# Optimization experiments

Hardware: AMD Instinct MI355X
Metric: run time of the kernel (lower is better)

Reference implementation:

```python
import jax, jax.numpy as jnp
import numpy as np
import math

B, T, H, NH, L = 8, 256, 128, 2, 2
DH = H // NH
KC = 3
ITEMNUM = 50000
TIME_SPAN = 256
PERIODS = jnp.array([86400.0, 604800.0, 2592000.0], dtype=jnp.float32)
SCALE_MAGS = [1.0, 1.0, 1.0]
NEG = -1e9


def layernorm(x, g, b, eps=1e-8):
    mu = x.mean(-1, keepdims=True)
    var = ((x - mu) ** 2).mean(-1, keepdims=True)
    return (x - mu) / jnp.sqrt(var + eps) * g + b


def time_encode(t, time_proj):
    # HarmonicTimeEncoding: [sin(2*pi*t/c), cos(2*pi*t/c)] per cycle -> Linear(2K->H, no bias)
    phase = 2.0 * math.pi * t[..., None] / PERIODS
    enc = jnp.concatenate([jnp.sin(phase), jnp.cos(phase)], axis=-1)  # (..., 2K)
    return enc @ time_proj.T


def phase_bias_fn(t, lambdas):
    # PhaseSimilarityBias: per-cycle cosine similarity of (sin,cos) phase vectors
    phase = 2.0 * math.pi * t[..., None] / PERIODS  # (B,T,K)
    phi = jnp.stack([jnp.sin(phase), jnp.cos(phase)], axis=-1)  # (B,T,K,2)
    phi = phi / jnp.maximum(jnp.linalg.norm(phi, axis=-1, keepdims=True), 1e-12)
    sim = jnp.einsum('btkd,bskd->btsk', phi, phi)
    return (sim * lambdas).sum(-1)  # (B,T,T)


def setup_inputs() -> dict:
    key = jax.random.key(0)
    ks = jax.random.split(key, 40)
    def n(i, shape, std=0.02):
        return jax.random.normal(ks[i], shape, dtype=jnp.float32) * std
    inp = {}
    inp['log_seqs'] = jax.random.randint(ks[0], (B, T), 0, ITEMNUM + 1)
    inp['time_matrices'] = jax.random.randint(ks[1], (B, T, T), 0, TIME_SPAN + 1)
    inp['time_seq'] = jnp.sort(jax.random.uniform(ks[2], (B, T), dtype=jnp.float32) * 5e6, axis=-1)
    inp['pos_seqs'] = jax.random.randint(ks[3], (B, T), 1, ITEMNUM + 1)
    inp['neg_seqs'] = jax.random.randint(ks[4], (B, T), 1, ITEMNUM + 1)
    inp['target_times'] = jax.random.uniform(ks[5], (B,), dtype=jnp.float32) * 5e6
    inp['item_emb'] = n(6, (ITEMNUM + 1, H)).at[0].set(0.0)  # padding_idx=0
    inp['abs_pos_K'] = n(7, (T, H))
    inp['abs_pos_V'] = n(8, (T, H))
    inp['time_K_emb'] = n(9, (TIME_SPAN + 1, H))
    inp['time_V_emb'] = n(10, (TIME_SPAN + 1, H))
    inp['Wq'] = n(11, (L, H, H), 0.05); inp['bq'] = jnp.zeros((L, H))
    inp['Wk'] = n(12, (L, H, H), 0.05); inp['bk'] = jnp.zeros((L, H))
    inp['Wv'] = n(13, (L, H, H), 0.05); inp['bv'] = jnp.zeros((L, H))
    inp['attn_ln_g'] = jnp.ones((L, H)); inp['attn_ln_b'] = jnp.zeros((L, H))
    inp['fwd_ln_g'] = jnp.ones((L, H)); inp['fwd_ln_b'] = jnp.zeros((L, H))
    inp['w1'] = n(14, (L, H, H), 0.05); inp['b1'] = jnp.zeros((L, H))
    inp['w2'] = n(15, (L, H, H), 0.05); inp['b2'] = jnp.zeros((L, H))
    inp['last_ln_g'] = jnp.ones((H,)); inp['last_ln_b'] = jnp.zeros((H,))
    inp['time_proj'] = n(16, (H, 2 * KC), 1.0 / math.sqrt(H))
    inp['lambdas'] = jnp.array(SCALE_MAGS, dtype=jnp.float32)
    inp['pred_W'] = n(17, (H, H), 0.05)
    inp['fus_W1'] = n(18, (H, 2 * H), 0.05); inp['fus_b1'] = jnp.zeros((H,))
    inp['fus_W2'] = n(19, (H, H), 0.05); inp['fus_b2'] = jnp.zeros((H,))
    return inp


def reference(log_seqs, time_matrices, time_seq, pos_seqs, neg_seqs, target_times,
              item_emb, abs_pos_K, abs_pos_V, time_K_emb, time_V_emb,
              Wq, bq, Wk, bk, Wv, bv, attn_ln_g, attn_ln_b, fwd_ln_g, fwd_ln_b,
              w1, b1, w2, b2, last_ln_g, last_ln_b, time_proj, lambdas,
              pred_W, fus_W1, fus_b1, fus_W2, fus_b2):
    seqs = item_emb[log_seqs] * math.sqrt(H)
    seqs = seqs + time_encode(time_seq, time_proj)
    tl_mask = (log_seqs == 0)  # (B,T) padding mask
    keep = (~tl_mask)[..., None].astype(seqs.dtype)
    seqs = seqs * keep
    absK = abs_pos_K.reshape(T, NH, DH).transpose(1, 0, 2)  # (NH,T,DH)
    absV = abs_pos_V.reshape(T, NH, DH).transpose(1, 0, 2)
    tK = time_K_emb[time_matrices].reshape(B, T, T, NH, DH)  # (B,T,T,NH,DH)
    tV = time_V_emb[time_matrices].reshape(B, T, T, NH, DH)
    pbias = phase_bias_fn(time_seq, lambdas)  # (B,T,T)
    causal = jnp.triu(jnp.ones((T, T), dtype=bool), k=1)
    mask = causal[None, None] | tl_mask[:, None, None, :]  # (B,1,T,T)
    for l in range(L):
        Qn = layernorm(seqs, attn_ln_g[l], attn_ln_b[l])
        q = (Qn @ Wq[l].T + bq[l]).reshape(B, T, NH, DH).transpose(0, 2, 1, 3)
        k = (seqs @ Wk[l].T + bk[l]).reshape(B, T, NH, DH).transpose(0, 2, 1, 3)
        v = (seqs @ Wv[l].T + bv[l]).reshape(B, T, NH, DH).transpose(0, 2, 1, 3)
        scores = jnp.einsum('bhqd,bhkd->bhqk', q, k)
        scores = scores + jnp.einsum('bhqd,hkd->bhqk', q, absK)
        scores = scores + jnp.einsum('bqkhd,bhqd->bhqk', tK, q)  # relative time-interval term
        scores = scores / math.sqrt(DH) + pbias[:, None]  # phase-similarity logit bias
        scores = jnp.where(mask, NEG, scores)
        A = jax.nn.softmax(scores, axis=-1)
        out = jnp.einsum('bhqk,bhkd->bhqd', A, v)
        out = out + jnp.einsum('bhqk,hkd->bhqd', A, absV)
        out = out + jnp.einsum('bhqk,bqkhd->bhqd', A, tV)
        out = out.transpose(0, 2, 1, 3).reshape(B, T, H)
        seqs = Qn + out
        x = layernorm(seqs, fwd_ln_g[l], fwd_ln_b[l])
        seqs = jax.nn.relu(x @ w1[l].T + b1[l]) @ w2[l].T + b2[l] + x
        seqs = seqs * keep
    log_feats = layernorm(seqs, last_ln_g, last_ln_b)
    H_per = time_encode(target_times, time_proj) @ pred_W.T  # (B,H)
    H_per = jnp.broadcast_to(H_per[:, None], (B, T, H))
    cat = jnp.concatenate([log_feats, H_per], axis=-1)
    fused = jax.nn.gelu(cat @ fus_W1.T + fus_b1, approximate=False) @ fus_W2.T + fus_b2
    pos_logits = (fused * item_emb[pos_seqs]).sum(-1)
    neg_logits = (fused * item_emb[neg_seqs]).sum(-1)
    return (pos_logits, neg_logits)
```

## Files before the change

### kernel.cpp

```cpp
#include <hip/hip_runtime.h>
#include <math.h>

#define TT 256
#define HH 128

__device__ __forceinline__ void enc6(float t, float e[6]) {
  float x = 6.2831853071795864769f * t;
  float a0 = x / 86400.0f, a1 = x / 604800.0f, a2 = x / 2592000.0f;
  e[0] = sinf(a0); e[1] = sinf(a1); e[2] = sinf(a2);
  e[3] = cosf(a0); e[4] = cosf(a1); e[5] = cosf(a2);
}

__global__ __launch_bounds__(128) void embed_kernel(
    const int* __restrict__ log_seqs, const float* __restrict__ time_seq,
    const float* __restrict__ item_emb, const float* __restrict__ time_proj,
    float* __restrict__ seqs, float* __restrict__ sc6) {
  int row = blockIdx.x;
  int h = threadIdx.x;
  float t = time_seq[row];
  float e[6]; enc6(t, e);
  int idx = log_seqs[row];
  const float* tp = time_proj + h * 6;
  float val = item_emb[(size_t)idx * HH + h] * 11.313708498984761f;
  val += e[0]*tp[0] + e[1]*tp[1] + e[2]*tp[2] + e[3]*tp[3] + e[4]*tp[4] + e[5]*tp[5];
  seqs[(size_t)row * HH + h] = (idx != 0) ? val : 0.0f;
  if (h < 6) sc6[row * 6 + h] = e[h];
}

__global__ __launch_bounds__(128) void qkv_fused(
    const float* __restrict__ S,
    const float* __restrict__ Wq, const float* __restrict__ bq,
    const float* __restrict__ Wk, const float* __restrict__ bk,
    const float* __restrict__ Wv, const float* __restrict__ bv,
    const float* __restrict__ lng, const float* __restrict__ lnb,
    const float* __restrict__ absK, const float* __restrict__ absV,
    float* __restrict__ QN, float* __restrict__ QB,
    float* __restrict__ KT, float* __restrict__ VB) {
  int which = blockIdx.x >> 8;
  int m0 = (blockIdx.x & 255) * 8;
  int n = threadIdx.x;
  __shared__ float At[8][132];
  __shared__ float mu[8], rs[8];
  #pragma unroll
  for (int r = 0; r < 8; ++r) At[r][n] = S[(size_t)(m0 + r) * HH + n];
  __syncthreads();
  if (which == 0) {
    if (n < 64) {
      int r = n >> 3, sg = n & 7;
      float s = 0.f;
      #pragma unroll
      for (int i = 0; i < 16; ++i) s += At[r][sg * 16 + i];
      s += __shfl_xor(s, 1); s += __shfl_xor(s, 2); s += __shfl_xor(s, 4);
      if (sg == 0) mu[r] = s * (1.0f / HH);
    }
    __syncthreads();
    if (n < 64) {
      int r = n >> 3, sg = n & 7;
      float mm = mu[r], s = 0.f;
      #pragma unroll
      for (int i = 0; i < 16; ++i) { float d = At[r][sg*16+i] - mm; s += d * d; }
      s += __shfl_xor(s, 1); s += __shfl_xor(s, 2); s += __shfl_xor(s, 4);
      if (sg == 0) rs[r] = rsqrtf(s * (1.0f / HH) + 1e-8f);
    }
    __syncthreads();
    float gg = lng[n], bb = lnb[n];
    #pragma unroll
    for (int r = 0; r < 8; ++r) {
      float v = (At[r][n] - mu[r]) * rs[r] * gg + bb;
      At[r][n] = v;
      QN[(size_t)(m0 + r) * HH + n] = v;
    }
    __syncthreads();
  }
  const float* W    = which == 0 ? Wq : which == 1 ? Wk : Wv;
  const float* bias = which == 0 ? bq : which == 1 ? bk : bv;
  const float* addP = which == 1 ? absK : which == 2 ? absV : nullptr;
  float* dst        = which == 0 ? QB : which == 1 ? KT : VB;
  float acc[8];
  #pragma unroll
  for (int r = 0; r < 8; ++r) acc[r] = 0.f;
  const float* wr = W + (size_t)n * HH;
  for (int d = 0; d < HH; d += 4) {
    float4 w = *(const float4*)(wr + d);
    #pragma unroll
    for (int r = 0; r < 8; ++r) {
      float4 a = *(const float4*)(&At[r][d]);
      acc[r] = fmaf(a.x, w.x, fmaf(a.y, w.y, fmaf(a.z, w.z, fmaf(a.w, w.w, acc[r]))));
    }
  }
  float bn = bias[n];
  #pragma unroll
  for (int r = 0; r < 8; ++r) {
    int m = m0 + r;
    float v = acc[r] + bn;
    if (addP) v += addP[(size_t)(m & 255) * HH + n];
    if (which == 1) {
      int bb2 = m >> 8, t = m & 255, hh2 = n >> 6, dd = n & 63;
      dst[(((size_t)(bb2 * 2 + hh2) * 64) + dd) * 256 + t] = v;
    } else {
      dst[(size_t)m * HH + n] = v;
    }
  }
}

__global__ __launch_bounds__(256) void pkscb_kernel(
    const float* __restrict__ QB, const float* __restrict__ tKe,
    const int* __restrict__ tmat, const int* __restrict__ log_seqs,
    const float* __restrict__ sc6, const float* __restrict__ lambdas,
    float* __restrict__ SCB) {
  int blk = blockIdx.x;
  int qt = blk & 63, bh = blk >> 6;
  int h = bh & 1, b = bh >> 1;
  int q0 = qt << 2, hoff = h << 6;
  int tid = threadIdx.x;
  __shared__ float Qs[4][64];
  __shared__ float PKl[4][264];
  __shared__ float sk6T[6][256];
  __shared__ float sq6[4][6];
  __shared__ unsigned char kmask[256];
  { int q = tid >> 6, d = tid & 63;
    Qs[q][d] = QB[((size_t)(b * TT + q0 + q)) * HH + hoff + d]; }
  for (int idx = tid; idx < 1536; idx += 256) {
    int kk = idx / 6, cc = idx - kk * 6;
    sk6T[cc][kk] = sc6[(size_t)b * 1536 + idx];
  }
  if (tid < 24) {
    int q = tid / 6, cc = tid - q * 6;
    sq6[q][cc] = sc6[((size_t)(b * TT + q0 + q)) * 6 + cc];
  }
  kmask[tid] = (log_seqs[b * TT + tid] == 0) ? 1 : 0;
  __syncthreads();
  for (int i = tid; i < 257; i += 256) {
    const float* tp = tKe + (size_t)i * HH + hoff;
    float a0 = 0.f, a1 = 0.f, a2 = 0.f, a3 = 0.f;
    #pragma unroll
    for (int d = 0; d < 64; d += 4) {
      float4 t4 = *(const float4*)(tp + d);
      float4 v0 = *(const float4*)(&Qs[0][d]);
      float4 v1 = *(const float4*)(&Qs[1][d]);
      float4 v2 = *(const float4*)(&Qs[2][d]);
      float4 v3 = *(const float4*)(&Qs[3][d]);
      a0 = fmaf(v0.x,t4.x,fmaf(v0.y,t4.y,fmaf(v0.z,t4.z,fmaf(v0.w,t4.w,a0))));
      a1 = fmaf(v1.x,t4.x,fmaf(v1.y,t4.y,fmaf(v1.z,t4.z,fmaf(v1.w,t4.w,a1))));
      a2 = fmaf(v2.x,t4.x,fmaf(v2.y,t4.y,fmaf(v2.z,t4.z,fmaf(v2.w,t4.w,a2))));
      a3 = fmaf(v3.x,t4.x,fmaf(v3.y,t4.y,fmaf(v3.z,t4.z,fmaf(v3.w,t4.w,a3))));
    }
    PKl[0][i] = a0 * 0.125f; PKl[1][i] = a1 * 0.125f;
    PKl[2][i] = a2 * 0.125f; PKl[3][i] = a3 * 0.125f;
  }
  __syncthreads();
  float l0 = lambdas[0], l1 = lambdas[1], l2 = lambdas[2];
  int k = tid;
  float c0 = sk6T[0][k], c1 = sk6T[1][k], c2 = sk6T[2][k],
        c3 = sk6T[3][k], c4 = sk6T[4][k], c5 = sk6T[5][k];
  int km = kmask[k];
  float* scbq = SCB + ((size_t)(bh * TT + q0)) * TT;
  #pragma unroll
  for (int qq = 0; qq < 4; ++qq) {
    int qg = q0 + qq;
    float pb = l0 * (sq6[qq][0] * c0 + sq6[qq][3] * c3)
             + l1 * (sq6[qq][1] * c1 + sq6[qq][4] * c4)
             + l2 * (sq6[qq][2] * c2 + sq6[qq][5] * c5);
    int tm = tmat[((size_t)(b * TT + qg)) * TT + k];
    float val = (k > qg || km) ? -1e9f : (PKl[qq][tm] + pb);
    scbq[(size_t)qq * TT + k] = val;
  }
}

__global__ __launch_bounds__(256) void attn_fused(
    const float* __restrict__ QB, const float* __restrict__ KT,
    const float* __restrict__ VB, const float* __restrict__ QN,
    const float* __restrict__ SCB, const int* __restrict__ tmat,
    const float* __restrict__ tVe, float* __restrict__ out) {
  int blk = blockIdx.x;
  blk = (blk & 7) * 256 + (blk >> 3);
  int qt = blk & 127;
  int h = (blk >> 7) & 1;
  int b = blk >> 8;
  int q0 = qt << 1;
  int hoff = h << 6;
  int tid = threadIdx.x;
  int w = tid >> 6, lane = tid & 63;

  __shared__ float Qt[2][64];
  __shared__ float Pp[2][256];
  __shared__ unsigned short tmq[2][256];
  __shared__ float part[4][2][64];
  __shared__ float red[16];

  if (tid < 128)
    Qt[tid >> 6][tid & 63] = QB[((size_t)(b * TT + q0 + (tid >> 6))) * HH + hoff + (tid & 63)];
  #pragma unroll
  for (int t = 0; t < 2; ++t) {
    int idx = tid + t * 256;
    int qq = idx >> 8, kk = idx & 255;
    tmq[qq][kk] = (unsigned short)tmat[((size_t)(b * TT + q0 + qq)) * TT + kk];
  }
  __syncthreads();

  int k = (w << 6) | lane;
  const float* scb0 = SCB + ((size_t)((b * 2 + h) * TT + q0)) * TT;
  float s0 = scb0[k];
  float s1 = scb0[TT + k];
  if ((w << 6) <= q0 + 1) {
    float a0 = 0.f, a1 = 0.f;
    const float* ktb = KT + ((size_t)((b * 2 + h) * 64)) * 256 + k;
    #pragma unroll
    for (int d4 = 0; d4 < 16; ++d4) {
      float4 qa = *(const float4*)(&Qt[0][d4 << 2]);
      float4 qb = *(const float4*)(&Qt[1][d4 << 2]);
      const float* kp = ktb + (size_t)(d4 << 2) * 256;
      float v0 = kp[0], v1 = kp[256], v2 = kp[512], v3 = kp[768];
      a0 = fmaf(qa.x, v0, fmaf(qa.y, v1, fmaf(qa.z, v2, fmaf(qa.w, v3, a0))));
      a1 = fmaf(qb.x, v0, fmaf(qb.y, v1, fmaf(qb.z, v2, fmaf(qb.w, v3, a1))));
    }
    if (s0 > -5e8f) s0 = fmaf(a0, 0.125f, s0);
    if (s1 > -5e8f) s1 = fmaf(a1, 0.125f, s1);
  }
  float m0 = s0, m1 = s1;
  #pragma unroll
  for (int o = 32; o > 0; o >>= 1) {
    m0 = fmaxf(m0, __shfl_xor(m0, o));
    m1 = fmaxf(m1, __shfl_xor(m1, o));
  }
  if (lane == 0) { red[w] = m0; red[4 + w] = m1; }
  __syncthreads();
  float gm0 = fmaxf(fmaxf(red[0], red[1]), fmaxf(red[2], red[3]));
  float gm1 = fmaxf(fmaxf(red[4], red[5]), fmaxf(red[6], red[7]));
  float p0 = (gm0 < -5e8f) ? 1.0f : __expf(s0 - gm0);
  float p1 = (gm1 < -5e8f) ? 1.0f : __expf(s1 - gm1);
  float u0 = p0, u1 = p1;
  #pragma unroll
  for (int o = 32; o > 0; o >>= 1) {
    u0 += __shfl_xor(u0, o);
    u1 += __shfl_xor(u1, o);
  }
  if (lane == 0) { red[8 + w] = u0; red[12 + w] = u1; }
  __syncthreads();
  float inv0 = 1.0f / (red[8] + red[9] + red[10] + red[11]);
  float inv1 = 1.0f / (red[12] + red[13] + red[14] + red[15]);
  Pp[0][k] = p0 * inv0;
  Pp[1][k] = p1 * inv1;
  __syncthreads();

  int kend = (gm0 < -5e8f || gm1 < -5e8f) ? 256 : (q0 + 2);
  float o0 = 0.f, o1 = 0.f;
  const float* vbase = VB + ((size_t)(b * TT)) * HH + hoff + lane;
  const float* tvb   = tVe + hoff + lane;
  for (int kk = w; kk < kend; kk += 4) {
    float pa  = Pp[0][kk];
    float pb2 = Pp[1][kk];
    int ta = tmq[0][kk], tb = tmq[1][kk];
    float v  = vbase[(size_t)kk * HH];
    float t0 = tvb[(size_t)ta * HH];
    float t1 = tvb[(size_t)tb * HH];
    o0 = fmaf(pa,  v + t0, o0);
    o1 = fmaf(pb2, v + t1, o1);
  }
  part[w][0][lane] = o0;
  part[w][1][lane] = o1;
  __syncthreads();
  if (tid < 128) {
    int qq = tid >> 6, d = tid & 63;
    float o = part[0][qq][d] + part[1][qq][d] + part[2][qq][d] + part[3][qq][d];
    size_t ob = ((size_t)(b * TT + q0 + qq)) * HH + hoff + d;
    out[ob] = QN[ob] + o;
  }
}

__global__ __launch_bounds__(128) void ffn_fused(
    const float* __restrict__ S, const float* __restrict__ W1, const float* __restrict__ b1,
    const float* __restrict__ W2, const float* __restrict__ b2,
    const float* __restrict__ lng, const float* __restrict__ lnb,
    const int* __restrict__ log_seqs, float* __restrict__ outS) {
  int m0 = blockIdx.x * 4;
  int n = threadIdx.x;
  __shared__ float Xt[4][132];
  __shared__ float Ht[4][132];
  __shared__ float mu[4], rs[4];
  #pragma unroll
  for (int r = 0; r < 4; ++r) Xt[r][n] = S[(size_t)(m0 + r) * HH + n];
  __syncthreads();
  if (n < 32) {
    int r = n >> 3, sg = n & 7;
    float s = 0.f;
    #pragma unroll
    for (int i = 0; i < 16; ++i) s += Xt[r][sg * 16 + i];
    s += __shfl_xor(s, 1); s += __shfl_xor(s, 2); s += __shfl_xor(s, 4);
    if (sg == 0) mu[r] = s * (1.0f / HH);
  }
  __syncthreads();
  if (n < 32) {
    int r = n >> 3, sg = n & 7;
    float mm = mu[r], s = 0.f;
    #pragma unroll
    for (int i = 0; i < 16; ++i) { float d = Xt[r][sg*16+i] - mm; s += d * d; }
    s += __shfl_xor(s, 1); s += __shfl_xor(s, 2); s += __shfl_xor(s, 4);
    if (sg == 0) rs[r] = rsqrtf(s * (1.0f / HH) + 1e-8f);
  }
  __syncthreads();
  float gg = lng[n], bb = lnb[n];
  #pragma unroll
  for (int r = 0; r < 4; ++r) Xt[r][n] = (Xt[r][n] - mu[r]) * rs[r] * gg + bb;
  __syncthreads();
  float acc[4] = {0.f, 0.f, 0.f, 0.f};
  const float* wr = W1 + (size_t)n * HH;
  for (int d = 0; d < HH; d += 4) {
    float4 w = *(const float4*)(wr + d);
    #pragma unroll
    for (int r = 0; r < 4; ++r) {
      float4 a = *(const float4*)(&Xt[r][d]);
      acc[r] = fmaf(a.x, w.x, fmaf(a.y, w.y, fmaf(a.z, w.z, fmaf(a.w, w.w, acc[r]))));
    }
  }
  float b1n = b1[n];
  #pragma unroll
  for (int r = 0; r < 4; ++r) Ht[r][n] = fmaxf(acc[r] + b1n, 0.f);
  __syncthreads();
  float acc2[4] = {0.f, 0.f, 0.f, 0.f};
  wr = W2 + (size_t)n * HH;
  for (int d = 0; d < HH; d += 4) {
    float4 w = *(const float4*)(wr + d);
    #pragma unroll
    for (int r = 0; r < 4; ++r) {
      float4 a = *(const float4*)(&Ht[r][d]);
      acc2[r] = fmaf(a.x, w.x, fmaf(a.y, w.y, fmaf(a.z, w.z, fmaf(a.w, w.w, acc2[r]))));
    }
  }
  float b2n = b2[n];
  #pragma unroll
  for (int r = 0; r < 4; ++r) {
    int mrow = m0 + r;
    float v = acc2[r] + b2n + Xt[r][n];
    if (log_seqs[mrow] == 0) v = 0.f;
    outS[(size_t)mrow * HH + n] = v;
  }
}

__global__ __launch_bounds__(128) void hper_kernel(
    const float* __restrict__ target_t, const float* __restrict__ time_proj,
    const float* __restrict__ pred_W, const float* __restrict__ fus_W1,
    const float* __restrict__ fus_b1, float* __restrict__ hp1) {
  int b = blockIdx.x, hth = threadIdx.x;
  __shared__ float te[HH], hp[HH];
  float e[6]; enc6(target_t[b], e);
  const float* tp = time_proj + hth * 6;
  te[hth] = e[0]*tp[0]+e[1]*tp[1]+e[2]*tp[2]+e[3]*tp[3]+e[4]*tp[4]+e[5]*tp[5];
  __syncthreads();
  float u = 0.f;
  const float* pw = pred_W + (size_t)hth * HH;
  for (int d = 0; d < HH; ++d) u += te[d] * pw[d];
  hp[hth] = u;
  __syncthreads();
  float w = fus_b1[hth];
  const float* f1 = fus_W1 + (size_t)hth * 256 + 128;
  for (int d = 0; d < HH; ++d) w += hp[d] * f1[d];
  hp1[b * HH + hth] = w;
}

__global__ __launch_bounds__(128) void final_fused(
    const float* __restrict__ S, const float* __restrict__ lng, const float* __restrict__ lnb,
    const float* __restrict__ fus_W1, const float* __restrict__ HP1,
    const float* __restrict__ fus_W2, const float* __restrict__ fus_b2,
    const float* __restrict__ item_emb, const int* __restrict__ pos,
    const int* __restrict__ neg, float* __restrict__ out) {
  int m0 = blockIdx.x * 4;
  int bidx = m0 >> 8;
  int n = threadIdx.x;
  __shared__ float Xt[4][132];
  __shared__ float Ht[4][132];
  __shared__ float Ft[4][132];
  __shared__ float mu[4], rs[4];
  #pragma unroll
  for (int r = 0; r < 4; ++r) Xt[r][n] = S[(size_t)(m0 + r) * HH + n];
  __syncthreads();
  if (n < 32) {
    int r = n >> 3, sg = n & 7;
    float s = 0.f;
    #pragma unroll
    for (int i = 0; i < 16; ++i) s += Xt[r][sg * 16 + i];
    s += __shfl_xor(s, 1); s += __shfl_xor(s, 2); s += __shfl_xor(s, 4);
    if (sg == 0) mu[r] = s * (1.0f / HH);
  }
  __syncthreads();
  if (n < 32) {
    int r = n >> 3, sg = n & 7;
    float mm = mu[r], s = 0.f;
    #pragma unroll
    for (int i = 0; i < 16; ++i) { float d = Xt[r][sg*16+i] - mm; s += d * d; }
    s += __shfl_xor(s, 1); s += __shfl_xor(s, 2); s += __shfl_xor(s, 4);
    if (sg == 0) rs[r] = rsqrtf(s * (1.0f / HH) + 1e-8f);
  }
  __syncthreads();
  float gg = lng[n], bb = lnb[n];
  #pragma unroll
  for (int r = 0; r < 4; ++r) Xt[r][n] = (Xt[r][n] - mu[r]) * rs[r] * gg + bb;
  __syncthreads();
  float acc[4] = {0.f, 0.f, 0.f, 0.f};
  const float* wr = fus_W1 + (size_t)n * 256;
  for (int d = 0; d < HH; d += 4) {
    float4 w = *(const float4*)(wr + d);
    #pragma unroll
    for (int r = 0; r < 4; ++r) {
      float4 a = *(const float4*)(&Xt[r][d]);
      acc[r] = fmaf(a.x, w.x, fmaf(a.y, w.y, fmaf(a.z, w.z, fmaf(a.w, w.w, acc[r]))));
    }
  }
  float hp = HP1[bidx * HH + n];
  #pragma unroll
  for (int r = 0; r < 4; ++r) {
    float v = acc[r] + hp;
    Ht[r][n] = 0.5f * v * (1.0f + erff(v * 0.70710678118654752f));
  }
  __syncthreads();
  float acc2[4] = {0.f, 0.f, 0.f, 0.f};
  wr = fus_W2 + (size_t)n * HH;
  for (int d = 0; d < HH; d += 4) {
    float4 w = *(const float4*)(wr + d);
    #pragma unroll
    for (int r = 0; r < 4; ++r) {
      float4 a = *(const float4*)(&Ht[r][d]);
      acc2[r] = fmaf(a.x, w.x, fmaf(a.y, w.y, fmaf(a.z, w.z, fmaf(a.w, w.w, acc2[r]))));
    }
  }
  float b2n = fus_b2[n];
  #pragma unroll
  for (int r = 0; r < 4; ++r) Ft[r][n] = acc2[r] + b2n;
  __syncthreads();
  if (n < 64) {
    int task = n >> 3;
    int sg = n & 7;
    int r = task & 3;
    int w = task >> 2;
    int mrow = m0 + r;
    int idx = (w == 0) ? pos[mrow] : neg[mrow];
    const float* ie = item_emb + (size_t)idx * HH;
    float s = 0.f;
    #pragma unroll
    for (int i = 0; i < 16; ++i) s += Ft[r][sg * 16 + i] * ie[sg * 16 + i];
    s += __shfl_xor(s, 1); s += __shfl_xor(s, 2); s += __shfl_xor(s, 4);
    if (sg == 0) out[w * 2048 + mrow] = s;
  }
}

extern "C" void kernel_launch(void* const* d_in, const int* in_sizes, int n_in,
                              void* d_out, int out_size, void* d_ws, size_t ws_size,
                              hipStream_t stream) {
  const int*   log_seqs   = (const int*)d_in[0];
  const int*   tmat       = (const int*)d_in[1];
  const float* time_seq   = (const float*)d_in[2];
  const int*   pos_seqs   = (const int*)d_in[3];
  const int*   neg_seqs   = (const int*)d_in[4];
  const float* target_t   = (const float*)d_in[5];
  const float* item_emb   = (const float*)d_in[6];
  const float* abs_pos_K  = (const float*)d_in[7];
  const float* abs_pos_V  = (const float*)d_in[8];
  const float* time_K_emb = (const float*)d_in[9];
  const float* time_V_emb = (const float*)d_in[10];
  const float* Wq = (const float*)d_in[11];
  const float* bq = (const float*)d_in[12];
  const float* Wk = (const float*)d_in[13];
  const float* bk = (const float*)d_in[14];
  const float* Wv = (const float*)d_in[15];
  const float* bv = (const float*)d_in[16];
  const float* attn_ln_g = (const float*)d_in[17];
  const float* attn_ln_b = (const float*)d_in[18];
  const float* fwd_ln_g = (const float*)d_in[19];
  const float* fwd_ln_b = (const float*)d_in[20];
  const float* w1 = (const float*)d_in[21];
  const float* b1 = (const float*)d_in[22];
  const float* w2 = (const float*)d_in[23];
  const float* b2 = (const float*)d_in[24];
  const float* last_ln_g = (const float*)d_in[25];
  const float* last_ln_b = (const float*)d_in[26];
  const float* time_proj = (const float*)d_in[27];
  const float* lambdas = (const float*)d_in[28];
  const float* pred_W = (const float*)d_in[29];
  const float* fus_W1 = (const float*)d_in[30];
  const float* fus_b1 = (const float*)d_in[31];
  const float* fus_W2 = (const float*)d_in[32];
  const float* fus_b2 = (const float*)d_in[33];
  (void)in_sizes; (void)n_in; (void)out_size; (void)ws_size;

  float* out = (float*)d_out;
  float* ws = (float*)d_ws;
  const int M = 8 * TT;
  float* SC6  = ws;
  float* SEQS = SC6 + M * 6;
  float* QN   = SEQS + M * HH;
  float* QB   = QN + M * HH;
  float* KT   = QB + M * HH;
  float* VB   = KT + M * HH;
  float* HP1  = VB + M * HH;
  float* SCB  = HP1 + 8 * HH;

  embed_kernel<<<M, HH, 0, stream>>>(log_seqs, time_seq, item_emb, time_proj, SEQS, SC6);
  for (int l = 0; l < 2; ++l) {
    const size_t wo = (size_t)l * HH * HH;
    const size_t bo = (size_t)l * HH;
    qkv_fused<<<768, 128, 0, stream>>>(SEQS, Wq + wo, bq + bo, Wk + wo, bk + bo,
                                       Wv + wo, bv + bo, attn_ln_g + bo, attn_ln_b + bo,
                                       abs_pos_K, abs_pos_V, QN, QB, KT, VB);
    pkscb_kernel<<<1024, 256, 0, stream>>>(QB, time_K_emb, tmat, log_seqs, SC6, lambdas, SCB);
    attn_fused<<<2048, 256, 0, stream>>>(QB, KT, VB, QN, SCB, tmat, time_V_emb, SEQS);
    ffn_fused<<<512, 128, 0, stream>>>(SEQS, w1 + wo, b1 + bo, w2 + wo, b2 + bo,
                                       fwd_ln_g + bo, fwd_ln_b + bo, log_seqs, SEQS);
  }
  hper_kernel<<<8, 128, 0, stream>>>(target_t, time_proj, pred_W, fus_W1, fus_b1, HP1);
  final_fused<<<512, 128, 0, stream>>>(SEQS, last_ln_g, last_ln_b, fus_W1, HP1,
                                       fus_W2, fus_b2, item_emb, pos_seqs, neg_seqs, out);
}
```

Before: 294.5 us.

## Shrink row tiles in dense GEMM kernels and fold hper into embed kernel

The QKV, FFN and final fusion kernels now process 2 rows per 256-thread block instead of 4–8 rows per 128-thread block, giving many more blocks. LayerNorm uses wave-wide shuffle reductions in registers instead of a partial shared-memory pass. The small hper kernel is merged into the embedding launch as extra blocks, removing one launch. The aim is more parallelism and fewer launches, at the cost of less weight reuse per block, since each weight row is now read by twice as many blocks.

```diff
diff --git a/kernel.cpp b/kernel.cpp
--- a/kernel.cpp
+++ b/kernel.cpp
@@ -11,23 +11,49 @@
   e[3] = cosf(a0); e[4] = cosf(a1); e[5] = cosf(a2);
 }
 
-__global__ __launch_bounds__(128) void embed_kernel(
+__device__ __forceinline__ float wave_sum(float s) {
+  #pragma unroll
+  for (int o = 32; o > 0; o >>= 1) s += __shfl_xor(s, o);
+  return s;
+}
+
+__global__ __launch_bounds__(128) void embed_hper_kernel(
     const int* __restrict__ log_seqs, const float* __restrict__ time_seq,
     const float* __restrict__ item_emb, const float* __restrict__ time_proj,
-    float* __restrict__ seqs, float* __restrict__ sc6) {
-  int row = blockIdx.x;
-  int h = threadIdx.x;
-  float t = time_seq[row];
-  float e[6]; enc6(t, e);
-  int idx = log_seqs[row];
-  const float* tp = time_proj + h * 6;
-  float val = item_emb[(size_t)idx * HH + h] * 11.313708498984761f;
-  val += e[0]*tp[0] + e[1]*tp[1] + e[2]*tp[2] + e[3]*tp[3] + e[4]*tp[4] + e[5]*tp[5];
-  seqs[(size_t)row * HH + h] = (idx != 0) ? val : 0.0f;
-  if (h < 6) sc6[row * 6 + h] = e[h];
-}
-
-__global__ __launch_bounds__(128) void qkv_fused(
+    const float* __restrict__ target_t, const float* __restrict__ pred_W,
+    const float* __restrict__ fus_W1, const float* __restrict__ fus_b1,
+    float* __restrict__ seqs, float* __restrict__ sc6, float* __restrict__ hp1) {
+  int blk = blockIdx.x;
+  int tid = threadIdx.x;
+  if (blk < 2048) {
+    float t = time_seq[blk];
+    float e[6]; enc6(t, e);
+    int idx = log_seqs[blk];
+    const float* tp = time_proj + tid * 6;
+    float val = item_emb[(size_t)idx * HH + tid] * 11.313708498984761f;
+    val += e[0]*tp[0] + e[1]*tp[1] + e[2]*tp[2] + e[3]*tp[3] + e[4]*tp[4] + e[5]*tp[5];
+    seqs[(size_t)blk * HH + tid] = (idx != 0) ? val : 0.0f;
+    if (tid < 6) sc6[blk * 6 + tid] = e[tid];
+  } else {
+    int b = blk - 2048;
+    __shared__ float te[HH], hp[HH];
+    float e[6]; enc6(target_t[b], e);
+    const float* tp = time_proj + tid * 6;
+    te[tid] = e[0]*tp[0]+e[1]*tp[1]+e[2]*tp[2]+e[3]*tp[3]+e[4]*tp[4]+e[5]*tp[5];
+    __syncthreads();
+    float u = 0.f;
+    const float* pw = pred_W + (size_t)tid * HH;
+    for (int d = 0; d < HH; ++d) u += te[d] * pw[d];
+    hp[tid] = u;
+    __syncthreads();
+    float w = fus_b1[tid];
+    const float* f1 = fus_W1 + (size_t)tid * 256 + 128;
+    for (int d = 0; d < HH; ++d) w += hp[d] * f1[d];
+    hp1[b * HH + tid] = w;
+  }
+}
+
+__global__ __launch_bounds__(256) void qkv_gemm(
     const float* __restrict__ S,
     const float* __restrict__ Wq, const float* __restrict__ bq,
     const float* __restrict__ Wk, const float* __restrict__ bk,
@@ -36,70 +62,54 @@
     const float* __restrict__ absK, const float* __restrict__ absV,
     float* __restrict__ QN, float* __restrict__ QB,
     float* __restrict__ KT, float* __restrict__ VB) {
-  int which = blockIdx.x >> 8;
-  int m0 = (blockIdx.x & 255) * 8;
-  int n = threadIdx.x;
-  __shared__ float At[8][132];
-  __shared__ float mu[8], rs[8];
-  #pragma unroll
-  for (int r = 0; r < 8; ++r) At[r][n] = S[(size_t)(m0 + r) * HH + n];
-  __syncthreads();
+  int blk = blockIdx.x;
+  int which = blk >> 10;
+  int m0 = (blk & 1023) * 2;
+  int tid = threadIdx.x;
+  int r = tid >> 7, n = tid & 127, w = tid >> 6;
+  __shared__ float A2[2][HH];
+  __shared__ float red[8];
+  int m = m0 + r;
+  float x = S[(size_t)m * HH + n];
   if (which == 0) {
-    if (n < 64) {
-      int r = n >> 3, sg = n & 7;
-      float s = 0.f;
-      #pragma unroll
-      for (int i = 0; i < 16; ++i) s += At[r][sg * 16 + i];
-      s += __shfl_xor(s, 1); s += __shfl_xor(s, 2); s += __shfl_xor(s, 4);
-      if (sg == 0) mu[r] = s * (1.0f / HH);
-    }
+    float s = wave_sum(x);
+    if ((tid & 63) == 0) red[w] = s;
     __syncthreads();
-    if (n < 64) {
-      int r = n >> 3, sg = n & 7;
-      float mm = mu[r], s = 0.f;
-      #pragma unroll
-      for (int i = 0; i < 16; ++i) { float d = At[r][sg*16+i] - mm; s += d * d; }
-      s += __shfl_xor(s, 1); s += __shfl_xor(s, 2); s += __shfl_xor(s, 4);
-      if (sg == 0) rs[r] = rsqrtf(s * (1.0f / HH) + 1e-8f);
-    }
+    float mu = (red[r * 2] + red[r * 2 + 1]) * (1.0f / HH);
+    float dv = x - mu;
+    float v2 = wave_sum(dv * dv);
+    if ((tid & 63) == 0) red[4 + w] = v2;
     __syncthreads();
-    float gg = lng[n], bb = lnb[n];
-    #pragma unroll
-    for (int r = 0; r < 8; ++r) {
-      float v = (At[r][n] - mu[r]) * rs[r] * gg + bb;
-      At[r][n] = v;
-      QN[(size_t)(m0 + r) * HH + n] = v;
-    }
-    __syncthreads();
-  }
+    float var = (red[4 + r * 2] + red[5 + r * 2]) * (1.0f / HH);
+    x = dv * rsqrtf(var + 1e-8f) * lng[n] + lnb[n];
+    QN[(size_t)m * HH + n] = x;
+  }
+  A2[r][n] = x;
+  __syncthreads();
   const float* W    = which == 0 ? Wq : which == 1 ? Wk : Wv;
   const float* bias = which == 0 ? bq : which == 1 ? bk : bv;
-  const float* addP = which == 1 ? absK : which == 2 ? absV : nullptr;
-  float* dst        = which == 0 ? QB : which == 1 ? KT : VB;
-  float acc[8];
-  #pragma unroll
-  for (int r = 0; r < 8; ++r) acc[r] = 0.f;
   const float* wr = W + (size_t)n * HH;
-  for (int d = 0; d < HH; d += 4) {
-    float4 w = *(const float4*)(wr + d);
-    #pragma unroll
-    for (int r = 0; r < 8; ++r) {
-      float4 a = *(const float4*)(&At[r][d]);
-      acc[r] = fmaf(a.x, w.x, fmaf(a.y, w.y, fmaf(a.z, w.z, fmaf(a.w, w.w, acc[r]))));
-    }
-  }
-  float bn = bias[n];
-  #pragma unroll
-  for (int r = 0; r < 8; ++r) {
-    int m = m0 + r;
-    float v = acc[r] + bn;
-    if (addP) v += addP[(size_t)(m & 255) * HH + n];
-    if (which == 1) {
-      int bb2 = m >> 8, t = m & 255, hh2 = n >> 6, dd = n & 63;
-      dst[(((size_t)(bb2 * 2 + hh2) * 64) + dd) * 256 + t] = v;
-    } else {
-      dst[(size_t)m * HH + n] = v;
-    }
+  float acc0 = 0.f, acc1 = 0.f;
+  #pragma unroll
+  for (int d = 0; d < HH; d += 8) {
+    float4 w0 = *(const float4*)(wr + d);
+    float4 w1 = *(const float4*)(wr + d + 4);
+    float4 a0 = *(const float4*)(&A2[r][d]);
+    float4 a1 = *(const float4*)(&A2[r][d + 4]);
+    acc0 = fmaf(a0.x, w0.x, fmaf(a0.y, w0.y, fmaf(a0.z, w0.z, fmaf(a0.w, w0.w, acc0))));
+    acc1 = fmaf(a1.x, w1.x, fmaf(a1.y, w1.y, fmaf(a1.z, w1.z, fmaf(a1.w, w1.w, acc1))));
+  }
+  float v = acc0 + acc1 + bias[n];
+  int t = m & 255;
+  if (which == 0) {
+    QB[(size_t)m * HH + n] = v;
+  } else if (which == 1) {
+    v += absK[(size_t)t * HH + n];
+    int bb2 = m >> 8, hh2 = n >> 6, dd = n & 63;
+    KT[(((size_t)(bb2 * 2 + hh2) * 64) + dd) * 256 + t] = v;
+  } else {
+    v += absV[(size_t)t * HH + n];
+    VB[(size_t)m * HH + n] = v;
   }
 }
 
@@ -268,178 +278,132 @@
   }
 }
 
-__global__ __launch_bounds__(128) void ffn_fused(
+__global__ __launch_bounds__(256) void ffn_gemm(
     const float* __restrict__ S, const float* __restrict__ W1, const float* __restrict__ b1,
     const float* __restrict__ W2, const float* __restrict__ b2,
     const float* __restrict__ lng, const float* __restrict__ lnb,
     const int* __restrict__ log_seqs, float* __restrict__ outS) {
-  int m0 = blockIdx.x * 4;
-  int n = threadIdx.x;
-  __shared__ float Xt[4][132];
-  __shared__ float Ht[4][132];
-  __shared__ float mu[4], rs[4];
-  #pragma unroll
-  for (int r = 0; r < 4; ++r) Xt[r][n] = S[(size_t)(m0 + r) * HH + n];
-  __syncthreads();
-  if (n < 32) {
-    int r = n >> 3, sg = n & 7;
-    float s = 0.f;
-    #pragma unroll
-    for (int i = 0; i < 16; ++i) s += Xt[r][sg * 16 + i];
-    s += __shfl_xor(s, 1); s += __shfl_xor(s, 2); s += __shfl_xor(s, 4);
-    if (sg == 0) mu[r] = s * (1.0f / HH);
-  }
-  __syncthreads();
-  if (n < 32) {
-    int r = n >> 3, sg = n & 7;
-    float mm = mu[r], s = 0.f;
-    #pragma unroll
-    for (int i = 0; i < 16; ++i) { float d = Xt[r][sg*16+i] - mm; s += d * d; }
-    s += __shfl_xor(s, 1); s += __shfl_xor(s, 2); s += __shfl_xor(s, 4);
-    if (sg == 0) rs[r] = rsqrtf(s * (1.0f / HH) + 1e-8f);
-  }
-  __syncthreads();
-  float gg = lng[n], bb = lnb[n];
-  #pragma unroll
-  for (int r = 0; r < 4; ++r) Xt[r][n] = (Xt[r][n] - mu[r]) * rs[r] * gg + bb;
-  __syncthreads();
-  float acc[4] = {0.f, 0.f, 0.f, 0.f};
-  const float* wr = W1 + (size_t)n * HH;
-  for (int d = 0; d < HH; d += 4) {
-    float4 w = *(const float4*)(wr + d);
-    #pragma unroll
-    for (int r = 0; r < 4; ++r) {
-      float4 a = *(const float4*)(&Xt[r][d]);
-      acc[r] = fmaf(a.x, w.x, fmaf(a.y, w.y, fmaf(a.z, w.z, fmaf(a.w, w.w, acc[r]))));
-    }
-  }
-  float b1n = b1[n];
-  #pragma unroll
-  for (int r = 0; r < 4; ++r) Ht[r][n] = fmaxf(acc[r] + b1n, 0.f);
-  __syncthreads();
-  float acc2[4] = {0.f, 0.f, 0.f, 0.f};
-  wr = W2 + (size_t)n * HH;
-  for (int d = 0; d < HH; d += 4) {
-    float4 w = *(const float4*)(wr + d);
-    #pragma unroll
-    for (int r = 0; r < 4; ++r) {
-      float4 a = *(const float4*)(&Ht[r][d]);
-      acc2[r] = fmaf(a.x, w.x, fmaf(a.y, w.y, fmaf(a.z, w.z, fmaf(a.w, w.w, acc2[r]))));
-    }
-  }
-  float b2n = b2[n];
-  #pragma unroll
-  for (int r = 0; r < 4; ++r) {
-    int mrow = m0 + r;
-    float v = acc2[r] + b2n + Xt[r][n];
-    if (log_seqs[mrow] == 0) v = 0.f;
-    outS[(size_t)mrow * HH + n] = v;
-  }
-}
-
-__global__ __launch_bounds__(128) void hper_kernel(
-    const float* __restrict__ target_t, const float* __restrict__ time_proj,
-    const float* __restrict__ pred_W, const float* __restrict__ fus_W1,
-    const float* __restrict__ fus_b1, float* __restrict__ hp1) {
-  int b = blockIdx.x, hth = threadIdx.x;
-  __shared__ float te[HH], hp[HH];
-  float e[6]; enc6(target_t[b], e);
-  const float* tp = time_proj + hth * 6;
-  te[hth] = e[0]*tp[0]+e[1]*tp[1]+e[2]*tp[2]+e[3]*tp[3]+e[4]*tp[4]+e[5]*tp[5];
-  __syncthreads();
-  float u = 0.f;
-  const float* pw = pred_W + (size_t)hth * HH;
-  for (int d = 0; d < HH; ++d) u += te[d] * pw[d];
-  hp[hth] = u;
-  __syncthreads();
-  float w = fus_b1[hth];
-  const float* f1 = fus_W1 + (size_t)hth * 256 + 128;
-  for (int d = 0; d < HH; ++d) w += hp[d] * f1[d];
-  hp1[b * HH + hth] = w;
-}
-
-__global__ __launch_bounds__(128) void final_fused(
+  int m0 = blockIdx.x * 2;
+  int tid = threadIdx.x;
+  int r = tid >> 7, n = tid & 127, w = tid >> 6;
+  int m = m0 + r;
+  __shared__ float Xt[2][HH];
+  __shared__ float Ht[2][HH];
+  __shared__ float red[8];
+  float x = S[(size_t)m * HH + n];
+  float s = wave_sum(x);
+  if ((tid & 63) == 0) red[w] = s;
+  __syncthreads();
+  float mu = (red[r * 2] + red[r * 2 + 1]) * (1.0f / HH);
+  float dv = x - mu;
+  float v2 = wave_sum(dv * dv);
+  if ((tid & 63) == 0) red[4 + w] = v2;
+  __syncthreads();
+  float var = (red[4 + r * 2] + red[5 + r * 2]) * (1.0f / HH);
+  x = dv * rsqrtf(var + 1e-8f) * lng[n] + lnb[n];
+  Xt[r][n] = x;
+  __syncthreads();
+  {
+    const float* wr = W1 + (size_t)n * HH;
+    float acc0 = 0.f, acc1 = 0.f;
+    #pragma unroll
+    for (int d = 0; d < HH; d += 8) {
+      float4 w0 = *(const float4*)(wr + d);
+      float4 w1 = *(const float4*)(wr + d + 4);
+      float4 a0 = *(const float4*)(&Xt[r][d]);
+      float4 a1 = *(const float4*)(&Xt[r][d + 4]);
+      acc0 = fmaf(a0.x, w0.x, fmaf(a0.y, w0.y, fmaf(a0.z, w0.z, fmaf(a0.w, w0.w, acc0))));
+      acc1 = fmaf(a1.x, w1.x, fmaf(a1.y, w1.y, fmaf(a1.z, w1.z, fmaf(a1.w, w1.w, acc1))));
+    }
+    Ht[r][n] = fmaxf(acc0 + acc1 + b1[n], 0.f);
+  }
+  __syncthreads();
+  {
+    const float* wr = W2 + (size_t)n * HH;
+    float acc0 = 0.f, acc1 = 0.f;
+    #pragma unroll
+    for (int d = 0; d < HH; d += 8) {
+      float4 w0 = *(const float4*)(wr + d);
+      float4 w1 = *(const float4*)(wr + d + 4);
+      float4 a0 = *(const float4*)(&Ht[r][d]);
+      float4 a1 = *(const float4*)(&Ht[r][d + 4]);
+      acc0 = fmaf(a0.x, w0.x, fmaf(a0.y, w0.y, fmaf(a0.z, w0.z, fmaf(a0.w, w0.w, acc0))));
+      acc1 = fmaf(a1.x, w1.x, fmaf(a1.y, w1.y, fmaf(a1.z, w1.z, fmaf(a1.w, w1.w, acc1))));
+    }
+    float v = acc0 + acc1 + b2[n] + Xt[r][n];
+    if (log_seqs[m] == 0) v = 0.f;
+    outS[(size_t)m * HH + n] = v;
+  }
+}
+
+__global__ __launch_bounds__(256) void final_gemm(
     const float* __restrict__ S, const float* __restrict__ lng, const float* __restrict__ lnb,
     const float* __restrict__ fus_W1, const float* __restrict__ HP1,
     const float* __restrict__ fus_W2, const float* __restrict__ fus_b2,
     const float* __restrict__ item_emb, const int* __restrict__ pos,
     const int* __restrict__ neg, float* __restrict__ out) {
-  int m0 = blockIdx.x * 4;
+  int m0 = blockIdx.x * 2;
   int bidx = m0 >> 8;
-  int n = threadIdx.x;
-  __shared__ float Xt[4][132];
-  __shared__ float Ht[4][132];
-  __shared__ float Ft[4][132];
-  __shared__ float mu[4], rs[4];
-  #pragma unroll
-  for (int r = 0; r < 4; ++r) Xt[r][n] = S[(size_t)(m0 + r) * HH + n];
-  __syncthreads();
-  if (n < 32) {
-    int r = n >> 3, sg = n & 7;
-    float s = 0.f;
-    #pragma unroll
-    for (int i = 0; i < 16; ++i) s += Xt[r][sg * 16 + i];
-    s += __shfl_xor(s, 1); s += __shfl_xor(s, 2); s += __shfl_xor(s, 4);
-    if (sg == 0) mu[r] = s * (1.0f / HH);
-  }
-  __syncthreads();
-  if (n < 32) {
-    int r = n >> 3, sg = n & 7;
-    float mm = mu[r], s = 0.f;
-    #pragma unroll
-    for (int i = 0; i < 16; ++i) { float d = Xt[r][sg*16+i] - mm; s += d * d; }
-    s += __shfl_xor(s, 1); s += __shfl_xor(s, 2); s += __shfl_xor(s, 4);
-    if (sg == 0) rs[r] = rsqrtf(s * (1.0f / HH) + 1e-8f);
-  }
-  __syncthreads();
-  float gg = lng[n], bb = lnb[n];
-  #pragma unroll
-  for (int r = 0; r < 4; ++r) Xt[r][n] = (Xt[r][n] - mu[r]) * rs[r] * gg + bb;
-  __syncthreads();
-  float acc[4] = {0.f, 0.f, 0.f, 0.f};
-  const float* wr = fus_W1 + (size_t)n * 256;
-  for (int d = 0; d < HH; d += 4) {
-    float4 w = *(const float4*)(wr + d);
-    #pragma unroll
-    for (int r = 0; r < 4; ++r) {
-      float4 a = *(const float4*)(&Xt[r][d]);
-      acc[r] = fmaf(a.x, w.x, fmaf(a.y, w.y, fmaf(a.z, w.z, fmaf(a.w, w.w, acc[r]))));
-    }
-  }
-  float hp = HP1[bidx * HH + n];
-  #pragma unroll
-  for (int r = 0; r < 4; ++r) {
-    float v = acc[r] + hp;
+  int tid = threadIdx.x;
+  int r = tid >> 7, n = tid & 127, w = tid >> 6;
+  int lane = tid & 63;
+  int m = m0 + r;
+  __shared__ float Xt[2][HH];
+  __shared__ float Ht[2][HH];
+  __shared__ float Ft[2][HH];
+  __shared__ float red[8];
+  float x = S[(size_t)m * HH + n];
+  float s = wave_sum(x);
+  if ((tid & 63) == 0) red[w] = s;
+  __syncthreads();
+  float mu = (red[r * 2] + red[r * 2 + 1]) * (1.0f / HH);
+  float dv = x - mu;
+  float v2 = wave_sum(dv * dv);
+  if ((tid & 63) == 0) red[4 + w] = v2;
+  __syncthreads();
+  float var = (red[4 + r * 2] + red[5 + r * 2]) * (1.0f / HH);
+  Xt[r][n] = dv * rsqrtf(var + 1e-8f) * lng[n] + lnb[n];
+  __syncthreads();
+  {
+    const float* wr = fus_W1 + (size_t)n * 256;
+    float acc0 = 0.f, acc1 = 0.f;
+    #pragma unroll
+    for (int d = 0; d < HH; d += 8) {
+      float4 w0 = *(const float4*)(wr + d);
+      float4 w1 = *(const float4*)(wr + d + 4);
+      float4 a0 = *(const float4*)(&Xt[r][d]);
+      float4 a1 = *(const float4*)(&Xt[r][d + 4]);
+      acc0 = fmaf(a0.x, w0.x, fmaf(a0.y, w0.y, fmaf(a0.z, w0.z, fmaf(a0.w, w0.w, acc0))));
+      acc1 = fmaf(a1.x, w1.x, fmaf(a1.y, w1.y, fmaf(a1.z, w1.z, fmaf(a1.w, w1.w, acc1))));
+    }
+    float v = acc0 + acc1 + HP1[bidx * HH + n];
     Ht[r][n] = 0.5f * v * (1.0f + erff(v * 0.70710678118654752f));
   }
   __syncthreads();
-  float acc2[4] = {0.f, 0.f, 0.f, 0.f};
-  wr = fus_W2 + (size_t)n * HH;
-  for (int d = 0; d < HH; d += 4) {
-    float4 w = *(const float4*)(wr + d);
-    #pragma unroll
-    for (int r = 0; r < 4; ++r) {
-      float4 a = *(const float4*)(&Ht[r][d]);
-      acc2[r] = fmaf(a.x, w.x, fmaf(a.y, w.y, fmaf(a.z, w.z, fmaf(a.w, w.w, acc2[r]))));
-    }
-  }
-  float b2n = fus_b2[n];
-  #pragma unroll
-  for (int r = 0; r < 4; ++r) Ft[r][n] = acc2[r] + b2n;
-  __syncthreads();
-  if (n < 64) {
-    int task = n >> 3;
-    int sg = n & 7;
-    int r = task & 3;
-    int w = task >> 2;
-    int mrow = m0 + r;
-    int idx = (w == 0) ? pos[mrow] : neg[mrow];
+  {
+    const float* wr = fus_W2 + (size_t)n * HH;
+    float acc0 = 0.f, acc1 = 0.f;
+    #pragma unroll
+    for (int d = 0; d < HH; d += 8) {
+      float4 w0 = *(const float4*)(wr + d);
+      float4 w1 = *(const float4*)(wr + d + 4);
+      float4 a0 = *(const float4*)(&Ht[r][d]);
+      float4 a1 = *(const float4*)(&Ht[r][d + 4]);
+      acc0 = fmaf(a0.x, w0.x, fmaf(a0.y, w0.y, fmaf(a0.z, w0.z, fmaf(a0.w, w0.w, acc0))));
+      acc1 = fmaf(a1.x, w1.x, fmaf(a1.y, w1.y, fmaf(a1.z, w1.z, fmaf(a1.w, w1.w, acc1))));
+    }
+    Ft[r][n] = acc0 + acc1 + fus_b2[n];
+  }
+  __syncthreads();
+  {
+    int r2 = w & 1;
+    int pn = w >> 1;
+    int mrow = m0 + r2;
+    int idx = pn ? neg[mrow] : pos[mrow];
     const float* ie = item_emb + (size_t)idx * HH;
-    float s = 0.f;
-    #pragma unroll
-    for (int i = 0; i < 16; ++i) s += Ft[r][sg * 16 + i] * ie[sg * 16 + i];
-    s += __shfl_xor(s, 1); s += __shfl_xor(s, 2); s += __shfl_xor(s, 4);
-    if (sg == 0) out[w * 2048 + mrow] = s;
+    float sacc = Ft[r2][lane] * ie[lane] + Ft[r2][lane + 64] * ie[lane + 64];
+    sacc = wave_sum(sacc);
+    if (lane == 0) out[pn * 2048 + mrow] = sacc;
   }
 }
 
@@ -494,19 +458,20 @@
   float* HP1  = VB + M * HH;
   float* SCB  = HP1 + 8 * HH;
 
-  embed_kernel<<<M, HH, 0, stream>>>(log_seqs, time_seq, item_emb, time_proj, SEQS, SC6);
+  embed_hper_kernel<<<2056, 128, 0, stream>>>(log_seqs, time_seq, item_emb, time_proj,
+                                              target_t, pred_W, fus_W1, fus_b1,
+                                              SEQS, SC6, HP1);
   for (int l = 0; l < 2; ++l) {
     const size_t wo = (size_t)l * HH * HH;
     const size_t bo = (size_t)l * HH;
-    qkv_fused<<<768, 128, 0, stream>>>(SEQS, Wq + wo, bq + bo, Wk + wo, bk + bo,
+    qkv_gemm<<<3072, 256, 0, stream>>>(SEQS, Wq + wo, bq + bo, Wk + wo, bk + bo,
                                        Wv + wo, bv + bo, attn_ln_g + bo, attn_ln_b + bo,
                                        abs_pos_K, abs_pos_V, QN, QB, KT, VB);
     pkscb_kernel<<<1024, 256, 0, stream>>>(QB, time_K_emb, tmat, log_seqs, SC6, lambdas, SCB);
     attn_fused<<<2048, 256, 0, stream>>>(QB, KT, VB, QN, SCB, tmat, time_V_emb, SEQS);
-    ffn_fused<<<512, 128, 0, stream>>>(SEQS, w1 + wo, b1 + bo, w2 + wo, b2 + bo,
+    ffn_gemm<<<1024, 256, 0, stream>>>(SEQS, w1 + wo, b1 + bo, w2 + wo, b2 + bo,
                                        fwd_ln_g + bo, fwd_ln_b + bo, log_seqs, SEQS);
   }
-  hper_kernel<<<8, 128, 0, stream>>>(target_t, time_proj, pred_W, fus_W1, fus_b1, HP1);
-  final_fused<<<512, 128, 0, stream>>>(SEQS, last_ln_g, last_ln_b, fus_W1, HP1,
+  final_gemm<<<1024, 256, 0, stream>>>(SEQS, last_ln_g, last_ln_b, fus_W1, HP1,
                                        fus_W2, fus_b2, item_emb, pos_seqs, neg_seqs, out);
 }
```

Result: slower. 420.9 us (+42.9%).
